# Kernel optimization log

Hardware: AMD Instinct MI355X
Metric: run time of the kernel (lower is better)

The kernel has to match this reference:

```python
import jax, jax.numpy as jnp
import numpy as np

UNITS = 512
BACKCAST_LEN = 512
FORECAST_LEN = 128
NB_HARMONICS = 64  # forecast_length // 2
THETAS_DIM = 2 * NB_HARMONICS
BATCH = 16384


def _seasonality_basis(length, nb_harmonics):
    # t = 2*pi*arange(L)/L ; rows interleaved [cos(0*t), sin(0*t), cos(1*t), sin(1*t), ...]
    t = 2.0 * np.pi * jnp.arange(length, dtype=jnp.float32) / length
    i = jnp.arange(nb_harmonics, dtype=jnp.float32)[:, None]  # [H,1]
    angles = i * t[None, :]                                   # [H,L]
    basis = jnp.stack([jnp.cos(angles), jnp.sin(angles)], axis=1)  # [H,2,L]
    return basis.reshape(2 * nb_harmonics, length)            # [2H,L]


def setup_inputs() -> dict:
    key = jax.random.key(0)
    ks = jax.random.split(key, 10)
    s_in = 1.0 / np.sqrt(BACKCAST_LEN)
    s_u = 1.0 / np.sqrt(UNITS)
    return {
        "x": jax.random.normal(ks[0], (BATCH, BACKCAST_LEN), jnp.float32),
        "W1": jax.random.normal(ks[1], (UNITS, BACKCAST_LEN), jnp.float32) * s_in,
        "b1": jax.random.normal(ks[2], (UNITS,), jnp.float32) * s_in,
        "W2": jax.random.normal(ks[3], (UNITS, UNITS), jnp.float32) * s_u,
        "b2": jax.random.normal(ks[4], (UNITS,), jnp.float32) * s_u,
        "W3": jax.random.normal(ks[5], (UNITS, UNITS), jnp.float32) * s_u,
        "b3": jax.random.normal(ks[6], (UNITS,), jnp.float32) * s_u,
        "W4": jax.random.normal(ks[7], (UNITS, UNITS), jnp.float32) * s_u,
        "b4": jax.random.normal(ks[8], (UNITS,), jnp.float32) * s_u,
        "Wt": jax.random.normal(ks[9], (THETAS_DIM, UNITS), jnp.float32) * s_u,
    }


def reference(x, W1, b1, W2, b2, W3, b3, W4, b4, Wt):
    h = jax.nn.relu(x @ W1.T + b1)
    h = jax.nn.relu(h @ W2.T + b2)
    h = jax.nn.relu(h @ W3.T + b3)
    h = jax.nn.relu(h @ W4.T + b4)
    theta = h @ Wt.T  # [B, 2H], shared thetas (share_thetas=True)
    basis_b = _seasonality_basis(BACKCAST_LEN, NB_HARMONICS)  # [2H, Lb]
    basis_f = _seasonality_basis(FORECAST_LEN, NB_HARMONICS)  # [2H, Lf]
    backcast = theta @ basis_b  # [B, Lb]
    forecast = theta @ basis_f  # [B, Lf]
    return (backcast, forecast)
```

## Files before the change

### kernel.cpp

```cpp
#include <hip/hip_runtime.h>
#include <hip/hip_bf16.h>
#include <math.h>


#define BATCH 16384
#define ROWS  64

typedef __bf16 bf16x8 __attribute__((ext_vector_type(8)));
typedef float  f32x4  __attribute__((ext_vector_type(4)));

__device__ __forceinline__ unsigned short f2bf(float f) {
  union { float f; unsigned u; } v; v.f = f;
  unsigned r = v.u + 0x7fff + ((v.u >> 16) & 1);
  return (unsigned short)(r >> 16);
}

__global__ __launch_bounds__(256) void prep_kernel(
    const float* __restrict__ W1, const float* __restrict__ W2,
    const float* __restrict__ W3, const float* __restrict__ W4,
    const float* __restrict__ Wt,
    unsigned short* __restrict__ W1p, unsigned short* __restrict__ W2p,
    unsigned short* __restrict__ W3p, unsigned short* __restrict__ W4p,
    unsigned short* __restrict__ Wtp,
    unsigned short* __restrict__ basp) {
  const int t = blockIdx.x * 256 + threadIdx.x;
  if (t < 139264) {
    const float* src; unsigned short* dst; int u;
    if (t < 131072) {
      const int w = t >> 15; u = t & 32767;
      src = (w == 0) ? W1 : (w == 1) ? W2 : (w == 2) ? W3 : W4;
      dst = (w == 0) ? W1p : (w == 1) ? W2p : (w == 2) ? W3p : W4p;
    } else {
      u = t - 131072; src = Wt; dst = Wtp;
    }
    const int lane = u & 63, ks = (u >> 6) & 15, cf = u >> 10;
    const int col = cf * 16 + (lane & 15);
    const int k0  = ks * 32 + (lane >> 4) * 8;
    const float4* s = (const float4*)(src + (size_t)col * 512 + k0);
    const float4 a = s[0], b = s[1];
    uint4 o;
    o.x = f2bf(a.x) | ((unsigned)f2bf(a.y) << 16);
    o.y = f2bf(a.z) | ((unsigned)f2bf(a.w) << 16);
    o.z = f2bf(b.x) | ((unsigned)f2bf(b.y) << 16);
    o.w = f2bf(b.z) | ((unsigned)f2bf(b.w) << 16);
    ((uint4*)dst)[u] = o;
  } else if (t < 149504) {
    const int u = t - 139264;
    const int lane = u & 63, ks = (u >> 6) & 3, cf = u >> 8;
    const int col = cf * 16 + (lane & 15);
    const int r0  = ks * 32 + (lane >> 4) * 8;
    int l, L;
    if (col < 512) { l = col; L = 512; } else { l = col - 512; L = 128; }
    const float w0 = 6.283185307179586f * (float)l / (float)L;
    unsigned short e[8];
#pragma unroll
    for (int i = 0; i < 8; ++i) {
      const int r = r0 + i;
      const float ang = (float)(r >> 1) * w0;
      e[i] = f2bf((r & 1) ? sinf(ang) : cosf(ang));
    }
    uint4 o;
    o.x = e[0] | ((unsigned)e[1] << 16);
    o.y = e[2] | ((unsigned)e[3] << 16);
    o.z = e[4] | ((unsigned)e[5] << 16);
    o.w = e[6] | ((unsigned)e[7] << 16);
    ((uint4*)basp)[u] = o;
  }
}

__device__ __forceinline__ void wait_lds_and_barrier() {
  asm volatile("s_waitcnt lgkmcnt(0)" ::: "memory");
  __builtin_amdgcn_sched_barrier(0);
  __builtin_amdgcn_s_barrier();
  __builtin_amdgcn_sched_barrier(0);
}

template <int PHASE, bool PF_NEXT>
__device__ __forceinline__ void layer512(
    const unsigned short* hin, unsigned short* hout,
    const bf16x8* __restrict__ wcur, const bf16x8* __restrict__ wnext,
    const float* __restrict__ bias, bf16x8 (&bv)[6][4],
    const int wv, const int lane) {
  const int l15 = lane & 15, g = lane >> 4;
  f32x4 acc[4][4];
#pragma unroll
  for (int m = 0; m < 4; ++m)
#pragma unroll
    for (int n = 0; n < 4; ++n) acc[m][n] = (f32x4){0.f, 0.f, 0.f, 0.f};

  float4 bias4[4];
#pragma unroll
  for (int n = 0; n < 4; ++n)
    bias4[n] = *(const float4*)(bias + wv * 64 + n * 16 + g * 4);

  int rb[4], am[4];
#pragma unroll
  for (int m = 0; m < 4; ++m) {
    const int row = m * 16 + l15;
    rb[m] = row * 1024;
    am[m] = (row & 7) << 4;
  }

#pragma unroll
  for (int ks = 0; ks < 16; ++ks) {
    if (ks < 11) {
#pragma unroll
      for (int n = 0; n < 4; ++n)
        bv[(PHASE + ks + 5) % 6][n] = wcur[n * 1024 + (ks + 5) * 64];
    } else if (PF_NEXT) {
#pragma unroll
      for (int n = 0; n < 4; ++n)
        bv[(PHASE + ks + 5) % 6][n] = wnext[n * 1024 + (ks - 11) * 64];
    }
    bf16x8 av[4];
    const int kb = ks * 64 + g * 16;
#pragma unroll
    for (int m = 0; m < 4; ++m)
      av[m] = *(const bf16x8*)((const char*)hin + rb[m] + (kb ^ am[m]));
    __builtin_amdgcn_s_setprio(1);
#pragma unroll
    for (int m = 0; m < 4; ++m)
#pragma unroll
      for (int n = 0; n < 4; ++n)
        acc[m][n] = __builtin_amdgcn_mfma_f32_16x16x32_bf16(
            bv[(PHASE + ks) % 6][n], av[m], acc[m][n], 0, 0, 0);
    __builtin_amdgcn_s_setprio(0);
  }

#pragma unroll
  for (int m = 0; m < 4; ++m) {
    const int row = m * 16 + l15;
    const int sw  = (row & 7) << 4;
#pragma unroll
    for (int n = 0; n < 4; ++n) {
      const float v0 = fmaxf(acc[m][n][0] + bias4[n].x, 0.f);
      const float v1 = fmaxf(acc[m][n][1] + bias4[n].y, 0.f);
      const float v2 = fmaxf(acc[m][n][2] + bias4[n].z, 0.f);
      const float v3 = fmaxf(acc[m][n][3] + bias4[n].w, 0.f);
      uint2 o;
      o.x = f2bf(v0) | ((unsigned)f2bf(v1) << 16);
      o.y = f2bf(v2) | ((unsigned)f2bf(v3) << 16);
      const int c0 = (wv * 64 + n * 16 + g * 4) * 2;
      *(uint2*)((char*)hout + row * 1024 + (c0 ^ sw)) = o;
    }
  }
  wait_lds_and_barrier();
}

__global__ __launch_bounds__(512, 2) void fused_nbeats(
    const float* __restrict__ x,
    const bf16x8* __restrict__ W1p, const float* __restrict__ b1,
    const bf16x8* __restrict__ W2p, const float* __restrict__ b2,
    const bf16x8* __restrict__ W3p, const float* __restrict__ b3,
    const bf16x8* __restrict__ W4p, const float* __restrict__ b4,
    const bf16x8* __restrict__ Wtp,
    const bf16x8* __restrict__ basp,
    float* __restrict__ out) {
  __shared__ __align__(16) unsigned short h0[ROWS * 512];
  __shared__ __align__(16) unsigned short h1[ROWS * 512];

  const int tid  = threadIdx.x;
  const int lane = tid & 63;
  const int wv   = tid >> 6;
  const int l15  = lane & 15, g = lane >> 4;
  const int r0   = blockIdx.x * ROWS;

  const bf16x8* w1 = W1p + (size_t)wv * 4096 + lane;
  const bf16x8* w2 = W2p + (size_t)wv * 4096 + lane;
  const bf16x8* w3 = W3p + (size_t)wv * 4096 + lane;
  const bf16x8* w4 = W4p + (size_t)wv * 4096 + lane;

  bf16x8 bv[6][4];
#pragma unroll
  for (int s = 0; s < 5; ++s)
#pragma unroll
    for (int n = 0; n < 4; ++n) bv[s][n] = w1[n * 1024 + s * 64];

  {
    const float4* xs = (const float4*)(x + (size_t)r0 * 512);
#pragma unroll
    for (int j = 0; j < 16; ++j) {
      const int f = tid + j * 512;
      const int row = f >> 7, c4 = f & 127;
      const float4 v = xs[f];
      uint2 o;
      o.x = f2bf(v.x) | ((unsigned)f2bf(v.y) << 16);
      o.y = f2bf(v.z) | ((unsigned)f2bf(v.w) << 16);
      *(uint2*)((char*)h0 + row * 1024 + ((c4 * 8) ^ ((row & 7) << 4))) = o;
    }
  }
  wait_lds_and_barrier();

  layer512<0, true >(h0, h1, w1, w2, b1, bv, wv, lane);
  layer512<4, true >(h1, h0, w2, w3, b2, bv, wv, lane);
  layer512<2, true >(h0, h1, w3, w4, b3, bv, wv, lane);
  layer512<0, false>(h1, h0, w4, (const bf16x8*)0, b4, bv, wv, lane);

  {
    const bf16x8* tb = Wtp + (size_t)wv * 1024 + lane;
    bf16x8 tv[16];
#pragma unroll
    for (int s = 0; s < 16; ++s) tv[s] = tb[s * 64];

    int rb[4], am[4];
#pragma unroll
    for (int m = 0; m < 4; ++m) {
      const int row = m * 16 + l15;
      rb[m] = row * 1024;
      am[m] = (row & 7) << 4;
    }
    f32x4 tacc[4];
#pragma unroll
    for (int m = 0; m < 4; ++m) tacc[m] = (f32x4){0.f, 0.f, 0.f, 0.f};
#pragma unroll
    for (int ks = 0; ks < 16; ++ks) {
      bf16x8 av[4];
      const int kb = ks * 64 + g * 16;
#pragma unroll
      for (int m = 0; m < 4; ++m)
        av[m] = *(const bf16x8*)((const char*)h0 + rb[m] + (kb ^ am[m]));
      __builtin_amdgcn_s_setprio(1);
#pragma unroll
      for (int m = 0; m < 4; ++m)
        tacc[m] = __builtin_amdgcn_mfma_f32_16x16x32_bf16(
            tv[ks], av[m], tacc[m], 0, 0, 0);
      __builtin_amdgcn_s_setprio(0);
    }
#pragma unroll
    for (int m = 0; m < 4; ++m) {
      const int row = m * 16 + l15;
      const int sw  = (row & 7) << 4;
      uint2 o;
      o.x = f2bf(tacc[m][0]) | ((unsigned)f2bf(tacc[m][1]) << 16);
      o.y = f2bf(tacc[m][2]) | ((unsigned)f2bf(tacc[m][3]) << 16);
      const int c0 = (wv * 16 + g * 4) * 2;
      *(uint2*)((char*)h1 + row * 256 + (c0 ^ sw)) = o;
    }
  }
  wait_lds_and_barrier();

  {
    const bf16x8* bb = basp + (size_t)wv * 1280 + lane;
    bf16x8 bvv[5][4];
#pragma unroll
    for (int n = 0; n < 5; ++n)
#pragma unroll
      for (int ks = 0; ks < 4; ++ks) bvv[n][ks] = bb[n * 256 + ks * 64];

    f32x4 facc[4][5];
#pragma unroll
    for (int m = 0; m < 4; ++m)
#pragma unroll
      for (int n = 0; n < 5; ++n) facc[m][n] = (f32x4){0.f, 0.f, 0.f, 0.f};
    int rb2[4], am2[4];
#pragma unroll
    for (int m = 0; m < 4; ++m) {
      const int row = m * 16 + l15;
      rb2[m] = row * 256;
      am2[m] = (row & 7) << 4;
    }
#pragma unroll
    for (int ks = 0; ks < 4; ++ks) {
      bf16x8 av[4];
      const int kb = ks * 64 + g * 16;
#pragma unroll
      for (int m = 0; m < 4; ++m)
        av[m] = *(const bf16x8*)((const char*)h1 + rb2[m] + (kb ^ am2[m]));
      __builtin_amdgcn_s_setprio(1);
#pragma unroll
      for (int n = 0; n < 5; ++n)
#pragma unroll
        for (int m = 0; m < 4; ++m)
          facc[m][n] = __builtin_amdgcn_mfma_f32_16x16x32_bf16(
              bvv[n][ks], av[m], facc[m][n], 0, 0, 0);
      __builtin_amdgcn_s_setprio(0);
    }
#pragma unroll
    for (int n = 0; n < 5; ++n) {
      const int c0 = wv * 80 + n * 16 + g * 4;
#pragma unroll
      for (int m = 0; m < 4; ++m) {
        const int row = r0 + m * 16 + l15;
        float4 o = make_float4(facc[m][n][0], facc[m][n][1],
                               facc[m][n][2], facc[m][n][3]);
        if (c0 < 512)
          *(float4*)(out + (size_t)row * 512 + c0) = o;
        else
          *(float4*)(out + (size_t)BATCH * 512 + (size_t)row * 128 + (c0 - 512)) = o;
      }
    }
  }
}

extern "C" void kernel_launch(void* const* d_in, const int* in_sizes, int n_in,
                              void* d_out, int out_size, void* d_ws, size_t ws_size,
                              hipStream_t stream) {
  const float* x  = (const float*)d_in[0];
  const float* W1 = (const float*)d_in[1];
  const float* b1 = (const float*)d_in[2];
  const float* W2 = (const float*)d_in[3];
  const float* b2 = (const float*)d_in[4];
  const float* W3 = (const float*)d_in[5];
  const float* b3 = (const float*)d_in[6];
  const float* W4 = (const float*)d_in[7];
  const float* b4 = (const float*)d_in[8];
  const float* Wt = (const float*)d_in[9];

  unsigned short* ws  = (unsigned short*)d_ws;
  unsigned short* W1p = ws;
  unsigned short* W2p = ws + 262144;
  unsigned short* W3p = ws + 524288;
  unsigned short* W4p = ws + 786432;
  unsigned short* Wtp = ws + 1048576;
  unsigned short* basp = ws + 1114112;

  prep_kernel<<<584, 256, 0, stream>>>(W1, W2, W3, W4, Wt,
                                       W1p, W2p, W3p, W4p, Wtp, basp);
  fused_nbeats<<<BATCH / ROWS, 512, 0, stream>>>(
      x, (const bf16x8*)W1p, b1, (const bf16x8*)W2p, b2,
      (const bf16x8*)W3p, b3, (const bf16x8*)W4p, b4,
      (const bf16x8*)Wtp, (const bf16x8*)basp, (float*)d_out);
}
```

Before: 153.2 us.

## Overlap input load with first-layer MFMA and shrink weight prefetch ring

Splits the x tile load into two halves so the second half's global loads run while the first half's K-steps of layer 1 execute. It also shrinks the per-wave weight register ring from 6 to 4 stages, hoists the basis-weight loads ahead of the theta GEMM, and streams Wt through a rotating buffer instead of preloading all 16 slices. The s_setprio hints are dropped and occupancy is pinned with waves_per_eu. The aim is to hide global-load latency and cut register pressure, at the cost of a shorter prefetch distance that may expose weight-load latency.

```diff
diff --git a/kernel.cpp b/kernel.cpp
--- a/kernel.cpp
+++ b/kernel.cpp
@@ -75,58 +75,41 @@
   __builtin_amdgcn_sched_barrier(0);
 }
 
-template <int PHASE, bool PF_NEXT>
-__device__ __forceinline__ void layer512(
-    const unsigned short* hin, unsigned short* hout,
-    const bf16x8* __restrict__ wcur, const bf16x8* __restrict__ wnext,
-    const float* __restrict__ bias, bf16x8 (&bv)[6][4],
+template <int KB, int KE, bool PF>
+__device__ __forceinline__ void layer_ksteps(
+    const unsigned short* hin, const bf16x8* __restrict__ wcur,
+    const bf16x8* __restrict__ wnext,
+    bf16x8 (&bv)[4][4], f32x4 (&acc)[4][4],
+    const int (&rb)[4], const int (&am)[4], const int g) {
+#pragma unroll
+  for (int ks = KB; ks < KE; ++ks) {
+    if (ks < 13) {
+#pragma unroll
+      for (int n = 0; n < 4; ++n)
+        bv[(ks + 3) & 3][n] = wcur[n * 1024 + (ks + 3) * 64];
+    } else if (PF) {
+#pragma unroll
+      for (int n = 0; n < 4; ++n)
+        bv[(ks + 3) & 3][n] = wnext[n * 1024 + (ks - 13) * 64];
+    }
+    bf16x8 av[4];
+    const int kb = ks * 64 + g * 16;
+#pragma unroll
+    for (int m = 0; m < 4; ++m)
+      av[m] = *(const bf16x8*)((const char*)hin + rb[m] + (kb ^ am[m]));
+#pragma unroll
+    for (int m = 0; m < 4; ++m)
+#pragma unroll
+      for (int n = 0; n < 4; ++n)
+        acc[m][n] = __builtin_amdgcn_mfma_f32_16x16x32_bf16(
+            bv[ks & 3][n], av[m], acc[m][n], 0, 0, 0);
+  }
+}
+
+__device__ __forceinline__ void layer_epilogue(
+    unsigned short* hout, const float4 (&bias4)[4], f32x4 (&acc)[4][4],
     const int wv, const int lane) {
   const int l15 = lane & 15, g = lane >> 4;
-  f32x4 acc[4][4];
-#pragma unroll
-  for (int m = 0; m < 4; ++m)
-#pragma unroll
-    for (int n = 0; n < 4; ++n) acc[m][n] = (f32x4){0.f, 0.f, 0.f, 0.f};
-
-  float4 bias4[4];
-#pragma unroll
-  for (int n = 0; n < 4; ++n)
-    bias4[n] = *(const float4*)(bias + wv * 64 + n * 16 + g * 4);
-
-  int rb[4], am[4];
-#pragma unroll
-  for (int m = 0; m < 4; ++m) {
-    const int row = m * 16 + l15;
-    rb[m] = row * 1024;
-    am[m] = (row & 7) << 4;
-  }
-
-#pragma unroll
-  for (int ks = 0; ks < 16; ++ks) {
-    if (ks < 11) {
-#pragma unroll
-      for (int n = 0; n < 4; ++n)
-        bv[(PHASE + ks + 5) % 6][n] = wcur[n * 1024 + (ks + 5) * 64];
-    } else if (PF_NEXT) {
-#pragma unroll
-      for (int n = 0; n < 4; ++n)
-        bv[(PHASE + ks + 5) % 6][n] = wnext[n * 1024 + (ks - 11) * 64];
-    }
-    bf16x8 av[4];
-    const int kb = ks * 64 + g * 16;
-#pragma unroll
-    for (int m = 0; m < 4; ++m)
-      av[m] = *(const bf16x8*)((const char*)hin + rb[m] + (kb ^ am[m]));
-    __builtin_amdgcn_s_setprio(1);
-#pragma unroll
-    for (int m = 0; m < 4; ++m)
-#pragma unroll
-      for (int n = 0; n < 4; ++n)
-        acc[m][n] = __builtin_amdgcn_mfma_f32_16x16x32_bf16(
-            bv[(PHASE + ks) % 6][n], av[m], acc[m][n], 0, 0, 0);
-    __builtin_amdgcn_s_setprio(0);
-  }
-
 #pragma unroll
   for (int m = 0; m < 4; ++m) {
     const int row = m * 16 + l15;
@@ -147,7 +130,16 @@
   wait_lds_and_barrier();
 }
 
-__global__ __launch_bounds__(512, 2) void fused_nbeats(
+__device__ __forceinline__ void zero_acc(f32x4 (&acc)[4][4]) {
+#pragma unroll
+  for (int m = 0; m < 4; ++m)
+#pragma unroll
+    for (int n = 0; n < 4; ++n) acc[m][n] = (f32x4){0.f, 0.f, 0.f, 0.f};
+}
+
+__global__ __launch_bounds__(512)
+__attribute__((amdgpu_waves_per_eu(2, 2)))
+void fused_nbeats(
     const float* __restrict__ x,
     const bf16x8* __restrict__ W1p, const float* __restrict__ b1,
     const bf16x8* __restrict__ W2p, const float* __restrict__ b2,
@@ -170,61 +162,121 @@
   const bf16x8* w3 = W3p + (size_t)wv * 4096 + lane;
   const bf16x8* w4 = W4p + (size_t)wv * 4096 + lane;
 
-  bf16x8 bv[6][4];
-#pragma unroll
-  for (int s = 0; s < 5; ++s)
+  int rb[4], am[4];
+#pragma unroll
+  for (int m = 0; m < 4; ++m) {
+    const int row = m * 16 + l15;
+    rb[m] = row * 1024;
+    am[m] = (row & 7) << 4;
+  }
+
+  bf16x8 bv[4][4];
+#pragma unroll
+  for (int s = 0; s < 3; ++s)
 #pragma unroll
     for (int n = 0; n < 4; ++n) bv[s][n] = w1[n * 1024 + s * 64];
 
-  {
-    const float4* xs = (const float4*)(x + (size_t)r0 * 512);
-#pragma unroll
-    for (int j = 0; j < 16; ++j) {
-      const int f = tid + j * 512;
-      const int row = f >> 7, c4 = f & 127;
-      const float4 v = xs[f];
+  const float4* xs = (const float4*)(x + (size_t)r0 * 512);
+
+#pragma unroll
+  for (int j = 0; j < 8; ++j) {
+    const int idx = tid + j * 512;
+    const int row = idx >> 6, c4 = idx & 63;
+    const float4 v = xs[row * 128 + c4];
+    uint2 o;
+    o.x = f2bf(v.x) | ((unsigned)f2bf(v.y) << 16);
+    o.y = f2bf(v.z) | ((unsigned)f2bf(v.w) << 16);
+    *(uint2*)((char*)h0 + row * 1024 + ((c4 * 8) ^ ((row & 7) << 4))) = o;
+  }
+  wait_lds_and_barrier();
+
+  f32x4 acc[4][4];
+  zero_acc(acc);
+  {
+    float4 xr[8];
+#pragma unroll
+    for (int j = 0; j < 8; ++j) {
+      const int idx = tid + j * 512;
+      const int row = idx >> 6, c4 = idx & 63;
+      xr[j] = xs[row * 128 + 64 + c4];
+    }
+    layer_ksteps<0, 8, false>(h0, w1, w1, bv, acc, rb, am, g);
+#pragma unroll
+    for (int j = 0; j < 8; ++j) {
+      const int idx = tid + j * 512;
+      const int row = idx >> 6, c4b = 64 + (idx & 63);
       uint2 o;
-      o.x = f2bf(v.x) | ((unsigned)f2bf(v.y) << 16);
-      o.y = f2bf(v.z) | ((unsigned)f2bf(v.w) << 16);
-      *(uint2*)((char*)h0 + row * 1024 + ((c4 * 8) ^ ((row & 7) << 4))) = o;
-    }
-  }
-  wait_lds_and_barrier();
-
-  layer512<0, true >(h0, h1, w1, w2, b1, bv, wv, lane);
-  layer512<4, true >(h1, h0, w2, w3, b2, bv, wv, lane);
-  layer512<2, true >(h0, h1, w3, w4, b3, bv, wv, lane);
-  layer512<0, false>(h1, h0, w4, (const bf16x8*)0, b4, bv, wv, lane);
-
-  {
+      o.x = f2bf(xr[j].x) | ((unsigned)f2bf(xr[j].y) << 16);
+      o.y = f2bf(xr[j].z) | ((unsigned)f2bf(xr[j].w) << 16);
+      *(uint2*)((char*)h0 + row * 1024 + ((c4b * 8) ^ ((row & 7) << 4))) = o;
+    }
+    wait_lds_and_barrier();
+  }
+  {
+    float4 bias4[4];
+#pragma unroll
+    for (int n = 0; n < 4; ++n)
+      bias4[n] = *(const float4*)(b1 + wv * 64 + n * 16 + g * 4);
+    layer_ksteps<8, 16, true>(h0, w1, w2, bv, acc, rb, am, g);
+    layer_epilogue(h1, bias4, acc, wv, lane);
+  }
+
+  {
+    float4 bias4[4];
+#pragma unroll
+    for (int n = 0; n < 4; ++n)
+      bias4[n] = *(const float4*)(b2 + wv * 64 + n * 16 + g * 4);
+    zero_acc(acc);
+    layer_ksteps<0, 16, true>(h1, w2, w3, bv, acc, rb, am, g);
+    layer_epilogue(h0, bias4, acc, wv, lane);
+  }
+  {
+    float4 bias4[4];
+#pragma unroll
+    for (int n = 0; n < 4; ++n)
+      bias4[n] = *(const float4*)(b3 + wv * 64 + n * 16 + g * 4);
+    zero_acc(acc);
+    layer_ksteps<0, 16, true>(h0, w3, w4, bv, acc, rb, am, g);
+    layer_epilogue(h1, bias4, acc, wv, lane);
+  }
+  {
+    float4 bias4[4];
+#pragma unroll
+    for (int n = 0; n < 4; ++n)
+      bias4[n] = *(const float4*)(b4 + wv * 64 + n * 16 + g * 4);
+    zero_acc(acc);
+    layer_ksteps<0, 16, false>(h1, w4, w4, bv, acc, rb, am, g);
+    layer_epilogue(h0, bias4, acc, wv, lane);
+  }
+
+  const bf16x8* bb = basp + (size_t)wv * 1280 + lane;
+  bf16x8 bvv[5][4];
+  {
+#pragma unroll
+    for (int n = 0; n < 5; ++n)
+#pragma unroll
+      for (int ks = 0; ks < 4; ++ks) bvv[n][ks] = bb[n * 256 + ks * 64];
+
     const bf16x8* tb = Wtp + (size_t)wv * 1024 + lane;
-    bf16x8 tv[16];
-#pragma unroll
-    for (int s = 0; s < 16; ++s) tv[s] = tb[s * 64];
-
-    int rb[4], am[4];
-#pragma unroll
-    for (int m = 0; m < 4; ++m) {
-      const int row = m * 16 + l15;
-      rb[m] = row * 1024;
-      am[m] = (row & 7) << 4;
-    }
+    bf16x8 tv[4];
+#pragma unroll
+    for (int s = 0; s < 3; ++s) tv[s] = tb[s * 64];
+
     f32x4 tacc[4];
 #pragma unroll
     for (int m = 0; m < 4; ++m) tacc[m] = (f32x4){0.f, 0.f, 0.f, 0.f};
 #pragma unroll
     for (int ks = 0; ks < 16; ++ks) {
+      if (ks < 13) tv[(ks + 3) & 3] = tb[(ks + 3) * 64];
       bf16x8 av[4];
       const int kb = ks * 64 + g * 16;
 #pragma unroll
       for (int m = 0; m < 4; ++m)
         av[m] = *(const bf16x8*)((const char*)h0 + rb[m] + (kb ^ am[m]));
-      __builtin_amdgcn_s_setprio(1);
 #pragma unroll
       for (int m = 0; m < 4; ++m)
         tacc[m] = __builtin_amdgcn_mfma_f32_16x16x32_bf16(
-            tv[ks], av[m], tacc[m], 0, 0, 0);
-      __builtin_amdgcn_s_setprio(0);
+            tv[ks & 3], av[m], tacc[m], 0, 0, 0);
     }
 #pragma unroll
     for (int m = 0; m < 4; ++m) {
@@ -240,40 +292,27 @@
   wait_lds_and_barrier();
 
   {
-    const bf16x8* bb = basp + (size_t)wv * 1280 + lane;
-    bf16x8 bvv[5][4];
-#pragma unroll
-    for (int n = 0; n < 5; ++n)
-#pragma unroll
-      for (int ks = 0; ks < 4; ++ks) bvv[n][ks] = bb[n * 256 + ks * 64];
-
     f32x4 facc[4][5];
 #pragma unroll
     for (int m = 0; m < 4; ++m)
 #pragma unroll
       for (int n = 0; n < 5; ++n) facc[m][n] = (f32x4){0.f, 0.f, 0.f, 0.f};
-    int rb2[4], am2[4];
-#pragma unroll
-    for (int m = 0; m < 4; ++m) {
-      const int row = m * 16 + l15;
-      rb2[m] = row * 256;
-      am2[m] = (row & 7) << 4;
-    }
+    int rb2[4];
+#pragma unroll
+    for (int m = 0; m < 4; ++m) rb2[m] = (m * 16 + l15) * 256;
 #pragma unroll
     for (int ks = 0; ks < 4; ++ks) {
       bf16x8 av[4];
       const int kb = ks * 64 + g * 16;
 #pragma unroll
       for (int m = 0; m < 4; ++m)
-        av[m] = *(const bf16x8*)((const char*)h1 + rb2[m] + (kb ^ am2[m]));
-      __builtin_amdgcn_s_setprio(1);
+        av[m] = *(const bf16x8*)((const char*)h1 + rb2[m] + (kb ^ am[m]));
 #pragma unroll
       for (int n = 0; n < 5; ++n)
 #pragma unroll
         for (int m = 0; m < 4; ++m)
           facc[m][n] = __builtin_amdgcn_mfma_f32_16x16x32_bf16(
               bvv[n][ks], av[m], facc[m][n], 0, 0, 0);
-      __builtin_amdgcn_s_setprio(0);
     }
 #pragma unroll
     for (int n = 0; n < 5; ++n) {
```

Result: slower. 162.4 us (+6.0%).
